# Optimization experiments

Hardware: AMD Instinct MI355X
Metric: run time of the kernel (lower is better)

The kernel has to match this reference:

```python
import jax, jax.numpy as jnp
import numpy as np

T, B, C = 2048, 4, 512
H, K, P = 16, 31, 15  # num_heads, kernel_size, padding_l
R = C // H


def setup_inputs() -> dict:
    key = jax.random.key(0)
    ks = jax.random.split(key, 6)
    x = jax.random.normal(ks[0], (T, B, C), dtype=jnp.float32)
    s = 0.02
    W1 = jax.random.normal(ks[1], (C, C), dtype=jnp.float32) * s   # linear1 weight
    b1 = jnp.zeros((C,), dtype=jnp.float32)
    Wl = jax.random.normal(ks[2], (H * K, C), dtype=jnp.float32) * s  # weight_linear (no bias)
    W2 = jax.random.normal(ks[3], (C, C), dtype=jnp.float32) * s   # linear2 weight
    b2 = jnp.zeros((C,), dtype=jnp.float32)
    return {"x": x, "W1": W1, "b1": b1, "Wl": Wl, "W2": W2, "b2": b2}


def _dynamic_conv(h, Wl):
    # h: (T, B, C). Generate per-position per-head filters, softmax over K,
    # then banded weighted sum over a local window of K timesteps.
    w = jnp.einsum('tbc,kc->tbk', h, Wl).reshape(T, B, H, K)
    w = jax.nn.softmax(w, axis=-1)                      # weight_softmax=True
    # pad left P, right K-1-P ("same" window: position t sees h[t-P : t-P+K])
    hp = jnp.pad(h, ((P, K - 1 - P), (0, 0), (0, 0)))   # (T+K-1, B, C)
    idx = jnp.arange(T)[:, None] + jnp.arange(K)[None, :]  # (T, K)
    hw = hp[idx].reshape(T, K, B, H, R)                 # unfolded windows
    return jnp.einsum('tkbhr,tbhk->tbhr', hw, w).reshape(T, B, C)


def reference(x, W1, b1, Wl, W2, b2):
    h = jnp.einsum('tbc,dc->tbd', x, W1) + b1           # linear1 (glu=False -> no act)
    out = _dynamic_conv(h, Wl)                          # conv_bias=False
    out = jnp.einsum('tbc,dc->tbd', out, W2) + b2       # linear2
    return out
```

## Files before the change

kernel.cpp:

```cpp
#include <hip/hip_runtime.h>
#include <hip/hip_bf16.h>

#define TT 2048
#define BB 4
#define CC 512
#define HH 16
#define KK 31
#define PP 15
#define MM (TT*BB)
#define NPAD 512

typedef __bf16 bf16x8 __attribute__((ext_vector_type(8)));
typedef float f32x4 __attribute__((ext_vector_type(4)));
typedef unsigned short ushort8 __attribute__((ext_vector_type(8)));
typedef unsigned short ushort4v __attribute__((ext_vector_type(4)));

__device__ __forceinline__ float bf2f(unsigned short u) {
    return __uint_as_float(((unsigned int)u) << 16);
}
__device__ __forceinline__ unsigned short f2bf(float f) {
    unsigned int x = __float_as_uint(f);
    x += 0x7fffu + ((x >> 16) & 1u);
    return (unsigned short)(x >> 16);
}

__global__ __launch_bounds__(256) void cast_x(const float* __restrict__ src,
                                              unsigned short* __restrict__ dst) {
    const int i = (blockIdx.x * 256 + threadIdx.x) * 4;
    const float4 v = *(const float4*)&src[i];
    ushort4v o = { f2bf(v.x), f2bf(v.y), f2bf(v.z), f2bf(v.w) };
    *(ushort4v*)&dst[i] = o;
}

__global__ __launch_bounds__(256) void cast_weights(const float* __restrict__ W1,
                                                    const float* __restrict__ Wl,
                                                    const float* __restrict__ W2,
                                                    unsigned short* __restrict__ W1b,
                                                    unsigned short* __restrict__ Wlb,
                                                    unsigned short* __restrict__ W2b) {
    const int b = blockIdx.x;
    const int i = (b & 255) * 1024 + threadIdx.x * 4;
    const float* src;
    unsigned short* dst;
    int n_src = 262144;
    if (b < 256)      { src = W1; dst = W1b; }
    else if (b < 512) { src = Wl; dst = Wlb; n_src = HH * KK * CC; }
    else              { src = W2; dst = W2b; }
    ushort4v o = {0, 0, 0, 0};
    if (i < n_src) {
        const float4 v = *(const float4*)&src[i];
        o[0] = f2bf(v.x); o[1] = f2bf(v.y); o[2] = f2bf(v.z); o[3] = f2bf(v.w);
    }
    *(ushort4v*)&dst[i] = o;
}

#define GBM 128
#define GBN 64
#define GBK 64
#define KC  512
#define NT  8

#define STAGE(kt, buf)                                                                         \
    do {                                                                                       \
        const int k0_ = (kt) * GBK;                                                            \
        _Pragma("unroll")                                                                      \
        for (int j = 0; j < 4; ++j)                                                            \
            __builtin_amdgcn_global_load_lds(                                                  \
                (const __attribute__((address_space(1))) void*)(gA[j] + k0_),                  \
                (__attribute__((address_space(3))) void*)(&As[buf][0] + j * 2048 + wv * 512),  \
                16, 0, 0);                                                                     \
        _Pragma("unroll")                                                                      \
        for (int j = 0; j < 2; ++j)                                                            \
            __builtin_amdgcn_global_load_lds(                                                  \
                (const __attribute__((address_space(1))) void*)(gB[j] + k0_),                  \
                (__attribute__((address_space(3))) void*)(&Bs[buf][0] + j * 2048 + wv * 512),  \
                16, 0, 0);                                                                     \
    } while (0)

template<bool OUT_BF16>
__global__ __launch_bounds__(256, 2) void gemm_nt_mfma(const unsigned short* __restrict__ A,
                                                       const unsigned short* __restrict__ B,
                                                       const float* __restrict__ bias,
                                                       void* __restrict__ Cout,
                                                       int N, int nn) {
    __shared__ short As[3][GBM * GBK];
    __shared__ short Bs[3][GBN * GBK];

    const int tid = threadIdx.x;
    const int l   = tid & 63;
    const int wv  = tid >> 6;
    const int wr  = wv >> 1;
    const int wc  = wv & 1;

    const int s  = (blockIdx.x & 7) * (gridDim.x >> 3) + (blockIdx.x >> 3);
    const int bm = (s / nn) * GBM;
    const int bn = (s % nn) * GBN;

    const unsigned short* gA[4];
    const unsigned short* gB[2];
    #pragma unroll
    for (int j = 0; j < 4; ++j) {
        const int idx16 = j * 256 + tid;
        const int r  = idx16 >> 3;
        const int sl = (idx16 & 7) ^ (r & 7);
        gA[j] = A + (size_t)(bm + r) * KC + sl * 8;
    }
    #pragma unroll
    for (int j = 0; j < 2; ++j) {
        const int idx16 = j * 256 + tid;
        const int r  = idx16 >> 3;
        const int sl = (idx16 & 7) ^ (r & 7);
        gB[j] = B + (size_t)(bn + r) * KC + sl * 8;
    }

    f32x4 acc[4][2] = {};

    const int lr = l & 15;
    const int ls = l >> 4;
    int offA[4][2], offB[2][2];
    #pragma unroll
    for (int mi = 0; mi < 4; ++mi) {
        const int r = wr * 64 + mi * 16 + lr;
        #pragma unroll
        for (int ks = 0; ks < 2; ++ks)
            offA[mi][ks] = r * 64 + (((ks * 4 + ls) ^ (r & 7)) * 8);
    }
    #pragma unroll
    for (int ni = 0; ni < 2; ++ni) {
        const int r = wc * 32 + ni * 16 + lr;
        #pragma unroll
        for (int ks = 0; ks < 2; ++ks)
            offB[ni][ks] = r * 64 + (((ks * 4 + ls) ^ (r & 7)) * 8);
    }

    STAGE(0, 0);
    STAGE(1, 1);

    #pragma unroll
    for (int kt = 0; kt < NT; ++kt) {
        if (kt < NT - 1) asm volatile("s_waitcnt vmcnt(6)" ::: "memory");
        else             asm volatile("s_waitcnt vmcnt(0)" ::: "memory");
        __builtin_amdgcn_s_barrier();
        if (kt + 2 < NT) STAGE(kt + 2, (kt + 2) % 3);

        const int cb = kt % 3;
        bf16x8 af[4][2], bfv[2][2];
        #pragma unroll
        for (int mi = 0; mi < 4; ++mi)
            #pragma unroll
            for (int ks = 0; ks < 2; ++ks)
                af[mi][ks] = *(const bf16x8*)&As[cb][offA[mi][ks]];
        #pragma unroll
        for (int ni = 0; ni < 2; ++ni)
            #pragma unroll
            for (int ks = 0; ks < 2; ++ks)
                bfv[ni][ks] = *(const bf16x8*)&Bs[cb][offB[ni][ks]];

        #pragma unroll
        for (int mi = 0; mi < 4; ++mi)
            #pragma unroll
            for (int ni = 0; ni < 2; ++ni)
                #pragma unroll
                for (int ks = 0; ks < 2; ++ks)
                    acc[mi][ni] = __builtin_amdgcn_mfma_f32_16x16x32_bf16(af[mi][ks], bfv[ni][ks], acc[mi][ni], 0, 0, 0);
    }

    #pragma unroll
    for (int mi = 0; mi < 4; ++mi) {
        const int row0 = bm + wr * 64 + mi * 16 + ls * 4;
        #pragma unroll
        for (int ni = 0; ni < 2; ++ni) {
            const int col = bn + wc * 32 + ni * 16 + lr;
            const float bv = bias ? bias[col] : 0.0f;
            #pragma unroll
            for (int j = 0; j < 4; ++j) {
                const float v = acc[mi][ni][j] + bv;
                if (OUT_BF16)
                    ((unsigned short*)Cout)[(size_t)(row0 + j) * N + col] = f2bf(v);
                else
                    ((float*)Cout)[(size_t)(row0 + j) * N + col] = v;
            }
        }
    }
}

__global__ __launch_bounds__(256) void dynconv_fused(const unsigned short* __restrict__ hb,
                                                     const unsigned short* __restrict__ logits,
                                                     unsigned short* __restrict__ cvb) {
    __shared__ float w_s[64][33];

    const int bid = blockIdx.x;
    const int t   = (bid & 7) * 256 + (bid >> 3);
    const int tid = threadIdx.x;

    {
        const int r = tid >> 2;
        const int q = tid & 3;
        const int b = r >> 4, hd = r & 15;
        const unsigned short* lp = logits + (size_t)(t * BB + b) * NPAD + hd * KK;
        float e[8];
        const int k0 = q * 8;
        const int kn = (q == 3) ? 7 : 8;
        float mx = -1e30f;
        #pragma unroll
        for (int j = 0; j < 8; ++j) {
            e[j] = (j < kn) ? bf2f(lp[k0 + j]) : -1e30f;
            mx = fmaxf(mx, e[j]);
        }
        mx = fmaxf(mx, __shfl_xor(mx, 1, 4));
        mx = fmaxf(mx, __shfl_xor(mx, 2, 4));
        float sm = 0.f;
        #pragma unroll
        for (int j = 0; j < 8; ++j) {
            e[j] = (j < kn) ? __expf(e[j] - mx) : 0.f;
            sm += e[j];
        }
        sm += __shfl_xor(sm, 1, 4);
        sm += __shfl_xor(sm, 2, 4);
        const float inv = 1.f / sm;
        #pragma unroll
        for (int j = 0; j < 8; ++j)
            if (j < kn) w_s[r][k0 + j] = e[j] * inv;
    }
    __syncthreads();

    const int c0 = (tid & 63) * 8;
    const int b  = tid >> 6;
    const int wrow = b * 16 + (c0 >> 5);
    float acc[8] = {};
    #pragma unroll
    for (int k = 0; k < KK; ++k) {
        const int tt = t - PP + k;
        if ((unsigned)tt >= TT) continue;
        const ushort8 hv = *(const ushort8*)&hb[(size_t)((tt * BB + b) * CC) + c0];
        const float wk = w_s[wrow][k];
        #pragma unroll
        for (int j = 0; j < 8; ++j) acc[j] = fmaf(bf2f(hv[j]), wk, acc[j]);
    }
    ushort8 o;
    #pragma unroll
    for (int j = 0; j < 8; ++j) o[j] = f2bf(acc[j]);
    *(ushort8*)&cvb[(size_t)((t * BB + b) * CC) + c0] = o;
}

extern "C" void kernel_launch(void* const* d_in, const int* in_sizes, int n_in,
                              void* d_out, int out_size, void* d_ws, size_t ws_size,
                              hipStream_t stream) {
    const float* x  = (const float*)d_in[0];
    const float* W1 = (const float*)d_in[1];
    const float* b1 = (const float*)d_in[2];
    const float* Wl = (const float*)d_in[3];
    const float* W2 = (const float*)d_in[4];
    const float* b2 = (const float*)d_in[5];
    float* out = (float*)d_out;

    unsigned short* xb  = (unsigned short*)d_ws;
    unsigned short* hb  = xb  + (size_t)MM * CC;
    unsigned short* cvb = hb  + (size_t)MM * CC;
    unsigned short* W1b = cvb + (size_t)MM * CC;
    unsigned short* Wlb = W1b + (size_t)CC * CC;
    unsigned short* W2b = Wlb + (size_t)NPAD * CC;
    unsigned short* lgb = W2b + (size_t)CC * CC;

    const int nxc = MM * CC;

    cast_x<<<nxc / 1024, 256, 0, stream>>>(x, xb);
    cast_weights<<<768, 256, 0, stream>>>(W1, Wl, W2, W1b, Wlb, W2b);

    const int nblk = (MM / GBM) * (CC / GBN);

    gemm_nt_mfma<true><<<nblk, 256, 0, stream>>>(xb, W1b, b1, hb, CC, CC / GBN);
    gemm_nt_mfma<true><<<nblk, 256, 0, stream>>>(hb, Wlb, nullptr, lgb, NPAD, NPAD / GBN);
    dynconv_fused<<<TT, 256, 0, stream>>>(hb, lgb, cvb);
    gemm_nt_mfma<false><<<nblk, 256, 0, stream>>>(cvb, W2b, b2, out, CC, CC / GBN);
}
```

Measured before the change: 55.66 us.

## Load GEMM B operand directly to registers; tile dynconv over four timesteps

The GEMM no longer stages the B tile through LDS. Each wave loads its B fragments straight from global memory into double-buffered registers one k-step ahead, and the vmcnt wait is adjusted to match. This cuts LDS traffic and shared-memory footprint, but adds redundant global loads of B across waves and more register pressure. The dynamic conv kernel now uses 64-thread blocks that each handle four consecutive timesteps of one batch, reusing every loaded h row across up to four outputs to reduce global reads of h, at the cost of fewer threads per block and serial per-thread softmax over 31 taps.

```diff
diff --git a/kernel.cpp b/kernel.cpp
--- a/kernel.cpp
+++ b/kernel.cpp
@@ -69,12 +69,33 @@
                 (const __attribute__((address_space(1))) void*)(gA[j] + k0_),                  \
                 (__attribute__((address_space(3))) void*)(&As[buf][0] + j * 2048 + wv * 512),  \
                 16, 0, 0);                                                                     \
-        _Pragma("unroll")                                                                      \
-        for (int j = 0; j < 2; ++j)                                                            \
-            __builtin_amdgcn_global_load_lds(                                                  \
-                (const __attribute__((address_space(1))) void*)(gB[j] + k0_),                  \
-                (__attribute__((address_space(3))) void*)(&Bs[buf][0] + j * 2048 + wv * 512),  \
-                16, 0, 0);                                                                     \
+    } while (0)
+
+#define LOADB(kt, pb)                                                                          \
+    do {                                                                                       \
+        _Pragma("unroll")                                                                      \
+        for (int ni = 0; ni < 2; ++ni)                                                         \
+            _Pragma("unroll")                                                                  \
+            for (int ks = 0; ks < 2; ++ks)                                                     \
+                pb[ni][ks] = *(const bf16x8*)(gBreg[ni] + (kt) * GBK + ks * 32);               \
+    } while (0)
+
+#define COMPUTE(pb)                                                                            \
+    do {                                                                                       \
+        bf16x8 af[4][2];                                                                       \
+        _Pragma("unroll")                                                                      \
+        for (int mi = 0; mi < 4; ++mi)                                                         \
+            _Pragma("unroll")                                                                  \
+            for (int ks = 0; ks < 2; ++ks)                                                     \
+                af[mi][ks] = *(const bf16x8*)&As[cb][offA[mi][ks]];                            \
+        _Pragma("unroll")                                                                      \
+        for (int mi = 0; mi < 4; ++mi)                                                         \
+            _Pragma("unroll")                                                                  \
+            for (int ni = 0; ni < 2; ++ni)                                                     \
+                _Pragma("unroll")                                                              \
+                for (int ks = 0; ks < 2; ++ks)                                                 \
+                    acc[mi][ni] = __builtin_amdgcn_mfma_f32_16x16x32_bf16(af[mi][ks],          \
+                                      pb[ni][ks], acc[mi][ni], 0, 0, 0);                       \
     } while (0)
 
 template<bool OUT_BF16>
@@ -84,7 +105,6 @@
                                                        void* __restrict__ Cout,
                                                        int N, int nn) {
     __shared__ short As[3][GBM * GBK];
-    __shared__ short Bs[3][GBN * GBK];
 
     const int tid = threadIdx.x;
     const int l   = tid & 63;
@@ -97,7 +117,6 @@
     const int bn = (s % nn) * GBN;
 
     const unsigned short* gA[4];
-    const unsigned short* gB[2];
     #pragma unroll
     for (int j = 0; j < 4; ++j) {
         const int idx16 = j * 256 + tid;
@@ -105,19 +124,18 @@
         const int sl = (idx16 & 7) ^ (r & 7);
         gA[j] = A + (size_t)(bm + r) * KC + sl * 8;
     }
-    #pragma unroll
-    for (int j = 0; j < 2; ++j) {
-        const int idx16 = j * 256 + tid;
-        const int r  = idx16 >> 3;
-        const int sl = (idx16 & 7) ^ (r & 7);
-        gB[j] = B + (size_t)(bn + r) * KC + sl * 8;
-    }
-
-    f32x4 acc[4][2] = {};
 
     const int lr = l & 15;
     const int ls = l >> 4;
-    int offA[4][2], offB[2][2];
+
+    const unsigned short* gBreg[2];
+    #pragma unroll
+    for (int ni = 0; ni < 2; ++ni)
+        gBreg[ni] = B + (size_t)(bn + wc * 32 + ni * 16 + lr) * KC + ls * 8;
+
+    f32x4 acc[4][2] = {};
+
+    int offA[4][2];
     #pragma unroll
     for (int mi = 0; mi < 4; ++mi) {
         const int r = wr * 64 + mi * 16 + lr;
@@ -125,44 +143,27 @@
         for (int ks = 0; ks < 2; ++ks)
             offA[mi][ks] = r * 64 + (((ks * 4 + ls) ^ (r & 7)) * 8);
     }
-    #pragma unroll
-    for (int ni = 0; ni < 2; ++ni) {
-        const int r = wc * 32 + ni * 16 + lr;
-        #pragma unroll
-        for (int ks = 0; ks < 2; ++ks)
-            offB[ni][ks] = r * 64 + (((ks * 4 + ls) ^ (r & 7)) * 8);
-    }
+
+    bf16x8 bq0[2][2], bq1[2][2];
 
     STAGE(0, 0);
+    LOADB(0, bq0);
     STAGE(1, 1);
 
     #pragma unroll
     for (int kt = 0; kt < NT; ++kt) {
-        if (kt < NT - 1) asm volatile("s_waitcnt vmcnt(6)" ::: "memory");
+        if (kt + 1 < NT) {
+            if (kt & 1) LOADB(kt + 1, bq0);
+            else        LOADB(kt + 1, bq1);
+        }
+        if (kt < NT - 1) asm volatile("s_waitcnt vmcnt(8)" ::: "memory");
         else             asm volatile("s_waitcnt vmcnt(0)" ::: "memory");
         __builtin_amdgcn_s_barrier();
         if (kt + 2 < NT) STAGE(kt + 2, (kt + 2) % 3);
 
         const int cb = kt % 3;
-        bf16x8 af[4][2], bfv[2][2];
-        #pragma unroll
-        for (int mi = 0; mi < 4; ++mi)
-            #pragma unroll
-            for (int ks = 0; ks < 2; ++ks)
-                af[mi][ks] = *(const bf16x8*)&As[cb][offA[mi][ks]];
-        #pragma unroll
-        for (int ni = 0; ni < 2; ++ni)
-            #pragma unroll
-            for (int ks = 0; ks < 2; ++ks)
-                bfv[ni][ks] = *(const bf16x8*)&Bs[cb][offB[ni][ks]];
-
-        #pragma unroll
-        for (int mi = 0; mi < 4; ++mi)
-            #pragma unroll
-            for (int ni = 0; ni < 2; ++ni)
-                #pragma unroll
-                for (int ks = 0; ks < 2; ++ks)
-                    acc[mi][ni] = __builtin_amdgcn_mfma_f32_16x16x32_bf16(af[mi][ks], bfv[ni][ks], acc[mi][ni], 0, 0, 0);
+        if (kt & 1) COMPUTE(bq1);
+        else        COMPUTE(bq0);
     }
 
     #pragma unroll
@@ -184,63 +185,61 @@
     }
 }
 
-__global__ __launch_bounds__(256) void dynconv_fused(const unsigned short* __restrict__ hb,
-                                                     const unsigned short* __restrict__ logits,
-                                                     unsigned short* __restrict__ cvb) {
+__global__ __launch_bounds__(64) void dynconv_fused(const unsigned short* __restrict__ hb,
+                                                    const unsigned short* __restrict__ lgb,
+                                                    unsigned short* __restrict__ cvb) {
     __shared__ float w_s[64][33];
 
     const int bid = blockIdx.x;
-    const int t   = (bid & 7) * 256 + (bid >> 3);
+    const int u   = (bid & 7) * 256 + (bid >> 3);
+    const int tg  = u >> 2;
+    const int b   = u & 3;
+    const int t0  = tg * 4;
     const int tid = threadIdx.x;
 
     {
-        const int r = tid >> 2;
-        const int q = tid & 3;
-        const int b = r >> 4, hd = r & 15;
-        const unsigned short* lp = logits + (size_t)(t * BB + b) * NPAD + hd * KK;
-        float e[8];
-        const int k0 = q * 8;
-        const int kn = (q == 3) ? 7 : 8;
+        const int dt = tid >> 4, hd = tid & 15;
+        const unsigned short* lp = lgb + (size_t)((t0 + dt) * BB + b) * NPAD + hd * KK;
+        float e[KK];
         float mx = -1e30f;
         #pragma unroll
-        for (int j = 0; j < 8; ++j) {
-            e[j] = (j < kn) ? bf2f(lp[k0 + j]) : -1e30f;
-            mx = fmaxf(mx, e[j]);
-        }
-        mx = fmaxf(mx, __shfl_xor(mx, 1, 4));
-        mx = fmaxf(mx, __shfl_xor(mx, 2, 4));
+        for (int k = 0; k < KK; ++k) { e[k] = bf2f(lp[k]); mx = fmaxf(mx, e[k]); }
         float sm = 0.f;
         #pragma unroll
-        for (int j = 0; j < 8; ++j) {
-            e[j] = (j < kn) ? __expf(e[j] - mx) : 0.f;
-            sm += e[j];
-        }
-        sm += __shfl_xor(sm, 1, 4);
-        sm += __shfl_xor(sm, 2, 4);
+        for (int k = 0; k < KK; ++k) { e[k] = __expf(e[k] - mx); sm += e[k]; }
         const float inv = 1.f / sm;
         #pragma unroll
-        for (int j = 0; j < 8; ++j)
-            if (j < kn) w_s[r][k0 + j] = e[j] * inv;
+        for (int k = 0; k < KK; ++k) w_s[tid][k] = e[k] * inv;
     }
     __syncthreads();
 
-    const int c0 = (tid & 63) * 8;
-    const int b  = tid >> 6;
-    const int wrow = b * 16 + (c0 >> 5);
-    float acc[8] = {};
-    #pragma unroll
-    for (int k = 0; k < KK; ++k) {
-        const int tt = t - PP + k;
+    const int c0 = tid * 8;
+    const int hd = tid >> 2;
+    float acc[4][8] = {};
+    #pragma unroll
+    for (int j = 0; j < 34; ++j) {
+        const int tt = t0 - PP + j;
         if ((unsigned)tt >= TT) continue;
         const ushort8 hv = *(const ushort8*)&hb[(size_t)((tt * BB + b) * CC) + c0];
-        const float wk = w_s[wrow][k];
-        #pragma unroll
-        for (int j = 0; j < 8; ++j) acc[j] = fmaf(bf2f(hv[j]), wk, acc[j]);
-    }
-    ushort8 o;
-    #pragma unroll
-    for (int j = 0; j < 8; ++j) o[j] = f2bf(acc[j]);
-    *(ushort8*)&cvb[(size_t)((t * BB + b) * CC) + c0] = o;
+        float hf[8];
+        #pragma unroll
+        for (int cc = 0; cc < 8; ++cc) hf[cc] = bf2f(hv[cc]);
+        #pragma unroll
+        for (int dt = 0; dt < 4; ++dt) {
+            const int k = j - dt;
+            if (k < 0 || k >= KK) continue;
+            const float wk = w_s[dt * 16 + hd][k];
+            #pragma unroll
+            for (int cc = 0; cc < 8; ++cc) acc[dt][cc] = fmaf(hf[cc], wk, acc[dt][cc]);
+        }
+    }
+    #pragma unroll
+    for (int dt = 0; dt < 4; ++dt) {
+        ushort8 o;
+        #pragma unroll
+        for (int cc = 0; cc < 8; ++cc) o[cc] = f2bf(acc[dt][cc]);
+        *(ushort8*)&cvb[(size_t)(((t0 + dt) * BB + b) * CC) + c0] = o;
+    }
 }
 
 extern "C" void kernel_launch(void* const* d_in, const int* in_sizes, int n_in,
@@ -271,6 +270,6 @@
 
     gemm_nt_mfma<true><<<nblk, 256, 0, stream>>>(xb, W1b, b1, hb, CC, CC / GBN);
     gemm_nt_mfma<true><<<nblk, 256, 0, stream>>>(hb, Wlb, nullptr, lgb, NPAD, NPAD / GBN);
-    dynconv_fused<<<TT, 256, 0, stream>>>(hb, lgb, cvb);
+    dynconv_fused<<<TT * BB / 4, 64, 0, stream>>>(hb, lgb, cvb);
     gemm_nt_mfma<false><<<nblk, 256, 0, stream>>>(cvb, W2b, b2, out, CC, CC / GBN);
 }
```

Measured after the change: 71.74 us. 28.9% more time.

## Compute four timesteps per block in dynconv to reuse loaded h rows

Applied to the files above, without the earlier changes.

The dynamic-conv kernel now gives each 64-thread block four consecutive timesteps of one batch element instead of one timestep across all batches. Each loaded h row is reused across up to four output timesteps, so it reads 34 rows instead of 4×31. Softmax is now computed serially by one thread per (timestep, head) over all 31 taps rather than split across four lanes with shuffles. The cost is a larger register footprint (a 4×8 accumulator and 31 exponentials per thread) and smaller blocks, which may hurt latency hiding.

```diff
diff --git a/kernel.cpp b/kernel.cpp
--- a/kernel.cpp
+++ b/kernel.cpp
@@ -184,63 +184,61 @@
     }
 }
 
-__global__ __launch_bounds__(256) void dynconv_fused(const unsigned short* __restrict__ hb,
-                                                     const unsigned short* __restrict__ logits,
-                                                     unsigned short* __restrict__ cvb) {
+__global__ __launch_bounds__(64) void dynconv_fused(const unsigned short* __restrict__ hb,
+                                                    const unsigned short* __restrict__ lgb,
+                                                    unsigned short* __restrict__ cvb) {
     __shared__ float w_s[64][33];
 
     const int bid = blockIdx.x;
-    const int t   = (bid & 7) * 256 + (bid >> 3);
+    const int u   = (bid & 7) * 256 + (bid >> 3);
+    const int tg  = u >> 2;
+    const int b   = u & 3;
+    const int t0  = tg * 4;
     const int tid = threadIdx.x;
 
     {
-        const int r = tid >> 2;
-        const int q = tid & 3;
-        const int b = r >> 4, hd = r & 15;
-        const unsigned short* lp = logits + (size_t)(t * BB + b) * NPAD + hd * KK;
-        float e[8];
-        const int k0 = q * 8;
-        const int kn = (q == 3) ? 7 : 8;
+        const int dt = tid >> 4, hd = tid & 15;
+        const unsigned short* lp = lgb + (size_t)((t0 + dt) * BB + b) * NPAD + hd * KK;
+        float e[KK];
         float mx = -1e30f;
         #pragma unroll
-        for (int j = 0; j < 8; ++j) {
-            e[j] = (j < kn) ? bf2f(lp[k0 + j]) : -1e30f;
-            mx = fmaxf(mx, e[j]);
-        }
-        mx = fmaxf(mx, __shfl_xor(mx, 1, 4));
-        mx = fmaxf(mx, __shfl_xor(mx, 2, 4));
+        for (int k = 0; k < KK; ++k) { e[k] = bf2f(lp[k]); mx = fmaxf(mx, e[k]); }
         float sm = 0.f;
         #pragma unroll
-        for (int j = 0; j < 8; ++j) {
-            e[j] = (j < kn) ? __expf(e[j] - mx) : 0.f;
-            sm += e[j];
-        }
-        sm += __shfl_xor(sm, 1, 4);
-        sm += __shfl_xor(sm, 2, 4);
+        for (int k = 0; k < KK; ++k) { e[k] = __expf(e[k] - mx); sm += e[k]; }
         const float inv = 1.f / sm;
         #pragma unroll
-        for (int j = 0; j < 8; ++j)
-            if (j < kn) w_s[r][k0 + j] = e[j] * inv;
+        for (int k = 0; k < KK; ++k) w_s[tid][k] = e[k] * inv;
     }
     __syncthreads();
 
-    const int c0 = (tid & 63) * 8;
-    const int b  = tid >> 6;
-    const int wrow = b * 16 + (c0 >> 5);
-    float acc[8] = {};
-    #pragma unroll
-    for (int k = 0; k < KK; ++k) {
-        const int tt = t - PP + k;
+    const int c0 = tid * 8;
+    const int hd = tid >> 2;
+    float acc[4][8] = {};
+    #pragma unroll
+    for (int j = 0; j < 34; ++j) {
+        const int tt = t0 - PP + j;
         if ((unsigned)tt >= TT) continue;
         const ushort8 hv = *(const ushort8*)&hb[(size_t)((tt * BB + b) * CC) + c0];
-        const float wk = w_s[wrow][k];
-        #pragma unroll
-        for (int j = 0; j < 8; ++j) acc[j] = fmaf(bf2f(hv[j]), wk, acc[j]);
-    }
-    ushort8 o;
-    #pragma unroll
-    for (int j = 0; j < 8; ++j) o[j] = f2bf(acc[j]);
-    *(ushort8*)&cvb[(size_t)((t * BB + b) * CC) + c0] = o;
+        float hf[8];
+        #pragma unroll
+        for (int cc = 0; cc < 8; ++cc) hf[cc] = bf2f(hv[cc]);
+        #pragma unroll
+        for (int dt = 0; dt < 4; ++dt) {
+            const int k = j - dt;
+            if (k < 0 || k >= KK) continue;
+            const float wk = w_s[dt * 16 + hd][k];
+            #pragma unroll
+            for (int cc = 0; cc < 8; ++cc) acc[dt][cc] = fmaf(hf[cc], wk, acc[dt][cc]);
+        }
+    }
+    #pragma unroll
+    for (int dt = 0; dt < 4; ++dt) {
+        ushort8 o;
+        #pragma unroll
+        for (int cc = 0; cc < 8; ++cc) o[cc] = f2bf(acc[dt][cc]);
+        *(ushort8*)&cvb[(size_t)(((t0 + dt) * BB + b) * CC) + c0] = o;
+    }
 }
 
 extern "C" void kernel_launch(void* const* d_in, const int* in_sizes, int n_in,
@@ -271,6 +269,6 @@
 
     gemm_nt_mfma<true><<<nblk, 256, 0, stream>>>(xb, W1b, b1, hb, CC, CC / GBN);
     gemm_nt_mfma<true><<<nblk, 256, 0, stream>>>(hb, Wlb, nullptr, lgb, NPAD, NPAD / GBN);
-    dynconv_fused<<<TT, 256, 0, stream>>>(hb, lgb, cvb);
+    dynconv_fused<<<TT * BB / 4, 64, 0, stream>>>(hb, lgb, cvb);
     gemm_nt_mfma<false><<<nblk, 256, 0, stream>>>(cvb, W2b, b2, out, CC, CC / GBN);
 }
```

New measurement: 54.03 us. 2.9% less time.
